# Optimization experiments

Hardware: AMD Instinct MI355X
Metric: run time of the kernel (lower is better)

The kernel has to match this reference:

```python
import jax, jax.numpy as jnp
import numpy as np

N_TOKENS = 32768
D_MODEL = 1024
TOT_EXPERT = 16
TOP_K = 2


def setup_inputs() -> dict:
    key = jax.random.key(0)
    k1, k2 = jax.random.split(key)
    inp = jax.random.normal(k1, (N_TOKENS, D_MODEL), dtype=jnp.float32)
    # nn.Linear(d_model, tot_expert, bias=False) weight: [tot_expert, d_model]
    W = jax.random.normal(k2, (TOT_EXPERT, D_MODEL), dtype=jnp.float32) * 0.02
    return {"inp": inp, "W": W}


def reference(inp, W):
    # gate logits: [N, E]
    logits = jnp.einsum('nd,ed->ne', inp, W)
    # top-k over experts (sorted order differs from torch sorted=False, but the
    # selected set and the downstream math are identical)
    top_k_logits, top_k_indices = jax.lax.top_k(logits, TOP_K)  # [N, K]
    # scatter top-k logits into a -inf buffer, then softmax over experts
    rows = jnp.arange(inp.shape[0])[:, None]
    router = jnp.full_like(logits, -jnp.inf).at[rows, top_k_indices].set(top_k_logits)
    router_probs = jax.nn.softmax(router, axis=-1)  # [N, E]
    # load-balance loss: f_i (no-grad expert selection freq) dot P_i (mean prob)
    f_i = jnp.zeros((TOT_EXPERT,), jnp.float32).at[top_k_indices.reshape(-1)].add(1.0) / inp.shape[0]
    P_i = jnp.mean(router_probs.astype(jnp.float32), axis=0)
    loss = jnp.sum(jax.lax.stop_gradient(f_i) * P_i) * TOT_EXPERT
    # gather the softmaxed scores of the selected experts
    top_k_scores = jnp.take_along_axis(router_probs, top_k_indices, axis=-1)  # [N, K]
    return top_k_indices, top_k_scores, loss
```

## Files before the change

### kernel.cpp

```cpp
#include <hip/hip_runtime.h>
#include <math.h>

#define N_TOKENS 32768
#define D_MODEL  1024
#define N_EXPERT 16
#define TPB      256
#define NBLK     1024
#define TOKS     32
#define BATCH    16
#define EP       (N_EXPERT + 1)

typedef float f32x4 __attribute__((ext_vector_type(4)));
typedef float f32x2 __attribute__((ext_vector_type(2)));

template<int CTRL>
static __device__ __forceinline__ float dpp_xor(float v) {
    return __int_as_float(__builtin_amdgcn_update_dpp(
        0, __float_as_int(v), CTRL, 0xF, 0xF, true));
}

static __device__ __forceinline__ float dot4pk(f32x4 x, f32x4 w) {
    f32x2 xl = __builtin_shufflevector(x, x, 0, 1);
    f32x2 xh = __builtin_shufflevector(x, x, 2, 3);
    f32x2 wl = __builtin_shufflevector(w, w, 0, 1);
    f32x2 wh = __builtin_shufflevector(w, w, 2, 3);
    f32x2 m, r;
    asm("v_pk_mul_f32 %0, %1, %2" : "=v"(m) : "v"(xl), "v"(wl));
    asm("v_pk_fma_f32 %0, %1, %2, %3" : "=v"(r) : "v"(xh), "v"(wh), "v"(m));
    return r.x + r.y;
}


__global__ __launch_bounds__(TPB)
__attribute__((amdgpu_waves_per_eu(4, 4)))
void gate_kernel(const float* __restrict__ inp,
                 const float* __restrict__ W,
                 float* __restrict__ out,
                 float* __restrict__ ws)
{
    const int tid  = threadIdx.x;
    const int wave = tid >> 6;
    const int lane = tid & 63;
    const int p    = lane & 15;
    const int d0   = wave * 256 + lane * 4;
    const int base = blockIdx.x * TOKS;

    f32x4 wreg[N_EXPERT];
    #pragma unroll
    for (int j = 0; j < N_EXPERT; ++j)
        wreg[j] = *reinterpret_cast<const f32x4*>(W + (j ^ p) * D_MODEL + d0);

    __shared__ float lds_part[2][BATCH][4][EP];
    __shared__ float lds_red[4][2][N_EXPERT];

    float cnt_acc = 0.f;
    float ps_acc  = 0.f;

    const float* xptr = inp + (size_t)base * D_MODEL + d0;

#define LOADX(xr, t) xr = *reinterpret_cast<const f32x4*>(xptr + (size_t)(t) * D_MODEL);

#define DOTOK(xv, slot, BUF) do { \
    float a0 =dot4pk(xv,wreg[0]),  a1 =dot4pk(xv,wreg[1]);  \
    float a2 =dot4pk(xv,wreg[2]),  a3 =dot4pk(xv,wreg[3]);  \
    float a4 =dot4pk(xv,wreg[4]),  a5 =dot4pk(xv,wreg[5]);  \
    float a6 =dot4pk(xv,wreg[6]),  a7 =dot4pk(xv,wreg[7]);  \
    float a8 =dot4pk(xv,wreg[8]),  a9 =dot4pk(xv,wreg[9]);  \
    float a10=dot4pk(xv,wreg[10]), a11=dot4pk(xv,wreg[11]); \
    float a12=dot4pk(xv,wreg[12]), a13=dot4pk(xv,wreg[13]); \
    float a14=dot4pk(xv,wreg[14]), a15=dot4pk(xv,wreg[15]); \
    float b0 = a0 + dpp_xor<0x128>(a8);  \
    float b1 = a1 + dpp_xor<0x128>(a9);  \
    float b2 = a2 + dpp_xor<0x128>(a10); \
    float b3 = a3 + dpp_xor<0x128>(a11); \
    float b4 = a4 + dpp_xor<0x128>(a12); \
    float b5 = a5 + dpp_xor<0x128>(a13); \
    float b6 = a6 + dpp_xor<0x128>(a14); \
    float b7 = a7 + dpp_xor<0x128>(a15); \
    float c0 = b0 + __shfl_xor(b4, 4); \
    float c1 = b1 + __shfl_xor(b5, 4); \
    float c2 = b2 + __shfl_xor(b6, 4); \
    float c3 = b3 + __shfl_xor(b7, 4); \
    float d0_ = c0 + dpp_xor<0x4E>(c2); \
    float d1_ = c1 + dpp_xor<0x4E>(c3); \
    float s0  = d0_ + dpp_xor<0xB1>(d1_); \
    s0 += __shfl_xor(s0, 16); \
    s0 += __shfl_xor(s0, 32); \
    if (lane < N_EXPERT) BUF[slot][wave][lane] = s0; \
} while (0)

#define PHASEB(BUF, TOKBASE) do { \
    const int tgrp = tid >> 4; \
    const int el   = tid & 15; \
    float v1 = BUF[tgrp][0][el] + BUF[tgrp][1][el] \
             + BUF[tgrp][2][el] + BUF[tgrp][3][el]; \
    int   i1 = el; \
    float v2 = -INFINITY; \
    int   i2 = 0; \
    _Pragma("unroll") \
    for (int m = 1; m <= 8; m <<= 1) { \
        float o1 = __shfl_xor(v1, m); \
        int  oi1 = __shfl_xor(i1, m); \
        float o2 = __shfl_xor(v2, m); \
        int  oi2 = __shfl_xor(i2, m); \
        bool afirst = (v1 > o1) || (v1 == o1 && i1 < oi1); \
        float c1v = afirst ? v1 : o1;   int c1i = afirst ? i1 : oi1; \
        float bv  = afirst ? o1 : v1;   int bi  = afirst ? oi1 : i1; \
        float sv  = afirst ? v2 : o2;   int si  = afirst ? i2 : oi2; \
        bool sgt  = (bv > sv) || (bv == sv && bi < si); \
        v1 = c1v; i1 = c1i; \
        v2 = sgt ? bv : sv;  i2 = sgt ? bi : si; \
    } \
    float tt = expf(v2 - v1); \
    float p1 = 1.f / (1.f + tt); \
    float p2 = tt * p1; \
    const int tok = (TOKBASE) + tgrp; \
    if (el == 0) { \
        *reinterpret_cast<float2*>(out + 2 * tok) = \
            make_float2((float)i1, (float)i2); \
        *reinterpret_cast<float2*>(out + 2 * N_TOKENS + 2 * tok) = \
            make_float2(p1, p2); \
    } \
    cnt_acc += (el == i1 ? 1.f : 0.f) + (el == i2 ? 1.f : 0.f); \
    ps_acc  += (el == i1 ? p1  : 0.f) + (el == i2 ? p2  : 0.f); \
} while (0)

    f32x4 x0, x1, x2, x3;

    LOADX(x0, 0) LOADX(x1, 1) LOADX(x2, 2) LOADX(x3, 3)
    for (int g = 0; g < 3; ++g) {
        const int t = g * 4;
        DOTOK(x0, t + 0, lds_part[0]); LOADX(x0, t + 4)
        DOTOK(x1, t + 1, lds_part[0]); LOADX(x1, t + 5)
        DOTOK(x2, t + 2, lds_part[0]); LOADX(x2, t + 6)
        DOTOK(x3, t + 3, lds_part[0]); LOADX(x3, t + 7)
    }
    DOTOK(x0, 12, lds_part[0]); LOADX(x0, 16)
    DOTOK(x1, 13, lds_part[0]); LOADX(x1, 17)
    DOTOK(x2, 14, lds_part[0]); LOADX(x2, 18)
    DOTOK(x3, 15, lds_part[0]); LOADX(x3, 19)

    __syncthreads();
    PHASEB(lds_part[0], base);

    for (int g = 0; g < 3; ++g) {
        const int t = 16 + g * 4;
        DOTOK(x0, (t + 0) & 15, lds_part[1]); LOADX(x0, t + 4)
        DOTOK(x1, (t + 1) & 15, lds_part[1]); LOADX(x1, t + 5)
        DOTOK(x2, (t + 2) & 15, lds_part[1]); LOADX(x2, t + 6)
        DOTOK(x3, (t + 3) & 15, lds_part[1]); LOADX(x3, t + 7)
    }
    DOTOK(x0, 12, lds_part[1]);
    DOTOK(x1, 13, lds_part[1]);
    DOTOK(x2, 14, lds_part[1]);
    DOTOK(x3, 15, lds_part[1]);

    __syncthreads();
    PHASEB(lds_part[1], base + 16);

    cnt_acc += __shfl_xor(cnt_acc, 16); cnt_acc += __shfl_xor(cnt_acc, 32);
    ps_acc  += __shfl_xor(ps_acc, 16);  ps_acc  += __shfl_xor(ps_acc, 32);
    if (lane < N_EXPERT) {
        lds_red[wave][0][lane] = cnt_acc;
        lds_red[wave][1][lane] = ps_acc;
    }
    __syncthreads();
    if (tid < 32) {
        const int el = tid & 15;
        const int which = tid >> 4;
        float v = lds_red[0][which][el] + lds_red[1][which][el]
                + lds_red[2][which][el] + lds_red[3][which][el];
        ws[blockIdx.x * 32 + tid] = v;
    }
#undef LOADX
#undef DOTOK
#undef PHASEB
}

__global__ __launch_bounds__(1024)
void loss_kernel(const float* __restrict__ ws, float* __restrict__ out)
{
    __shared__ float red[32][33];
    __shared__ float col[32];
    const int tid = threadIdx.x;
    const int c   = tid & 31;
    const int r   = tid >> 5;
    float s0 = 0.f, s1 = 0.f, s2 = 0.f, s3 = 0.f;
    #pragma unroll
    for (int k = 0; k < 32; k += 4) {
        s0 += ws[(size_t)(r + (k + 0) * 32) * 32 + c];
        s1 += ws[(size_t)(r + (k + 1) * 32) * 32 + c];
        s2 += ws[(size_t)(r + (k + 2) * 32) * 32 + c];
        s3 += ws[(size_t)(r + (k + 3) * 32) * 32 + c];
    }
    red[r][c] = (s0 + s1) + (s2 + s3);
    __syncthreads();
    if (tid < 32) {
        float t = 0.f;
        #pragma unroll
        for (int k = 0; k < 32; ++k) t += red[k][tid];
        col[tid] = t;
    }
    __syncthreads();
    if (tid == 0) {
        float sum = 0.f;
        #pragma unroll
        for (int e = 0; e < N_EXPERT; ++e)
            sum += col[e] * col[16 + e];
        out[4 * N_TOKENS] = sum * (float)N_EXPERT
                          / ((float)N_TOKENS * (float)N_TOKENS);
    }
}

extern "C" void kernel_launch(void* const* d_in, const int* in_sizes, int n_in,
                              void* d_out, int out_size, void* d_ws, size_t ws_size,
                              hipStream_t stream)
{
    const float* inp = (const float*)d_in[0];
    const float* W   = (const float*)d_in[1];
    float* out = (float*)d_out;
    float* ws  = (float*)d_ws;

    gate_kernel<<<NBLK, TPB, 0, stream>>>(inp, W, out, ws);
    loss_kernel<<<1, 1024, 0, stream>>>(ws, out);
}
```

Before: 39.20 us.

## Merge two half-batch phases into one LDS buffer with a single barrier

The LDS partial-sum buffer is enlarged to hold all 32 tokens, so the kernel runs one continuous dot-product loop and a single __syncthreads before both top-k phases, instead of two half passes each followed by a barrier. The main loop is made rolled (unroll disabled), and the output stores become nontemporal. This removes one block-wide barrier and the mid-loop stall, at the cost of more LDS per block and loop overhead from the rolled loop.

```diff
diff --git a/kernel.cpp b/kernel.cpp
--- a/kernel.cpp
+++ b/kernel.cpp
@@ -7,7 +7,6 @@
 #define TPB      256
 #define NBLK     1024
 #define TOKS     32
-#define BATCH    16
 #define EP       (N_EXPERT + 1)
 
 typedef float f32x4 __attribute__((ext_vector_type(4)));
@@ -50,7 +49,7 @@
     for (int j = 0; j < N_EXPERT; ++j)
         wreg[j] = *reinterpret_cast<const f32x4*>(W + (j ^ p) * D_MODEL + d0);
 
-    __shared__ float lds_part[2][BATCH][4][EP];
+    __shared__ float lds_part[TOKS][4][EP];
     __shared__ float lds_red[4][2][N_EXPERT];
 
     float cnt_acc = 0.f;
@@ -60,7 +59,7 @@
 
 #define LOADX(xr, t) xr = *reinterpret_cast<const f32x4*>(xptr + (size_t)(t) * D_MODEL);
 
-#define DOTOK(xv, slot, BUF) do { \
+#define DOTOK(xv, slot) do { \
     float a0 =dot4pk(xv,wreg[0]),  a1 =dot4pk(xv,wreg[1]);  \
     float a2 =dot4pk(xv,wreg[2]),  a3 =dot4pk(xv,wreg[3]);  \
     float a4 =dot4pk(xv,wreg[4]),  a5 =dot4pk(xv,wreg[5]);  \
@@ -86,14 +85,15 @@
     float s0  = d0_ + dpp_xor<0xB1>(d1_); \
     s0 += __shfl_xor(s0, 16); \
     s0 += __shfl_xor(s0, 32); \
-    if (lane < N_EXPERT) BUF[slot][wave][lane] = s0; \
+    if (lane < N_EXPERT) lds_part[slot][wave][lane] = s0; \
 } while (0)
 
-#define PHASEB(BUF, TOKBASE) do { \
+#define PHASEB(SLOT0, TOKBASE) do { \
     const int tgrp = tid >> 4; \
     const int el   = tid & 15; \
-    float v1 = BUF[tgrp][0][el] + BUF[tgrp][1][el] \
-             + BUF[tgrp][2][el] + BUF[tgrp][3][el]; \
+    const int slot = (SLOT0) + tgrp; \
+    float v1 = lds_part[slot][0][el] + lds_part[slot][1][el] \
+             + lds_part[slot][2][el] + lds_part[slot][3][el]; \
     int   i1 = el; \
     float v2 = -INFINITY; \
     int   i2 = 0; \
@@ -116,47 +116,33 @@
     float p2 = tt * p1; \
     const int tok = (TOKBASE) + tgrp; \
     if (el == 0) { \
-        *reinterpret_cast<float2*>(out + 2 * tok) = \
-            make_float2((float)i1, (float)i2); \
-        *reinterpret_cast<float2*>(out + 2 * N_TOKENS + 2 * tok) = \
-            make_float2(p1, p2); \
+        f32x2 iv; iv.x = (float)i1; iv.y = (float)i2; \
+        f32x2 pv; pv.x = p1; pv.y = p2; \
+        __builtin_nontemporal_store(iv, \
+            reinterpret_cast<f32x2*>(out + 2 * tok)); \
+        __builtin_nontemporal_store(pv, \
+            reinterpret_cast<f32x2*>(out + 2 * N_TOKENS + 2 * tok)); \
     } \
     cnt_acc += (el == i1 ? 1.f : 0.f) + (el == i2 ? 1.f : 0.f); \
     ps_acc  += (el == i1 ? p1  : 0.f) + (el == i2 ? p2  : 0.f); \
 } while (0)
 
     f32x4 x0, x1, x2, x3;
-
     LOADX(x0, 0) LOADX(x1, 1) LOADX(x2, 2) LOADX(x3, 3)
-    for (int g = 0; g < 3; ++g) {
+    #pragma clang loop unroll(disable)
+    for (int g = 0; g < 7; ++g) {
         const int t = g * 4;
-        DOTOK(x0, t + 0, lds_part[0]); LOADX(x0, t + 4)
-        DOTOK(x1, t + 1, lds_part[0]); LOADX(x1, t + 5)
-        DOTOK(x2, t + 2, lds_part[0]); LOADX(x2, t + 6)
-        DOTOK(x3, t + 3, lds_part[0]); LOADX(x3, t + 7)
-    }
-    DOTOK(x0, 12, lds_part[0]); LOADX(x0, 16)
-    DOTOK(x1, 13, lds_part[0]); LOADX(x1, 17)
-    DOTOK(x2, 14, lds_part[0]); LOADX(x2, 18)
-    DOTOK(x3, 15, lds_part[0]); LOADX(x3, 19)
-
-    __syncthreads();
-    PHASEB(lds_part[0], base);
-
-    for (int g = 0; g < 3; ++g) {
-        const int t = 16 + g * 4;
-        DOTOK(x0, (t + 0) & 15, lds_part[1]); LOADX(x0, t + 4)
-        DOTOK(x1, (t + 1) & 15, lds_part[1]); LOADX(x1, t + 5)
-        DOTOK(x2, (t + 2) & 15, lds_part[1]); LOADX(x2, t + 6)
-        DOTOK(x3, (t + 3) & 15, lds_part[1]); LOADX(x3, t + 7)
-    }
-    DOTOK(x0, 12, lds_part[1]);
-    DOTOK(x1, 13, lds_part[1]);
-    DOTOK(x2, 14, lds_part[1]);
-    DOTOK(x3, 15, lds_part[1]);
-
-    __syncthreads();
-    PHASEB(lds_part[1], base + 16);
+        DOTOK(x0, t + 0); LOADX(x0, t + 4)
+        DOTOK(x1, t + 1); LOADX(x1, t + 5)
+        DOTOK(x2, t + 2); LOADX(x2, t + 6)
+        DOTOK(x3, t + 3); LOADX(x3, t + 7)
+    }
+    DOTOK(x0, 28); DOTOK(x1, 29); DOTOK(x2, 30); DOTOK(x3, 31);
+
+    __syncthreads();
+
+    PHASEB(0,  base);
+    PHASEB(16, base + 16);
 
     cnt_acc += __shfl_xor(cnt_acc, 16); cnt_acc += __shfl_xor(cnt_acc, 32);
     ps_acc  += __shfl_xor(ps_acc, 16);  ps_acc  += __shfl_xor(ps_acc, 32);
```

After: 39.39 us. About the same (+0.5%).
